# Performance work log

Measured on AMD Instinct MI355X. Metric: run time of the kernel, lower is better.

Reference implementation:

```python
import jax, jax.numpy as jnp
import numpy as np

B, S, D, H = 2, 2048, 1024, 16
DK = D // H

def setup_inputs() -> dict:
    key = jax.random.key(0)
    k_x, k_q, k_k, k_v, k_o = jax.random.split(key, 5)
    return {
        "x": jax.random.normal(k_x, (B, S, D), dtype=jnp.float32),
        "wq": jax.random.normal(k_q, (D, D), dtype=jnp.float32) * 0.02,
        "wk": jax.random.normal(k_k, (D, D), dtype=jnp.float32) * 0.02,
        "wv": jax.random.normal(k_v, (D, D), dtype=jnp.float32) * 0.02,
        "wo": jax.random.normal(k_o, (D, D), dtype=jnp.float32) * 0.02,
    }

def reference(x, wq, wk, wv, wo):
    b, s, d = x.shape
    # project and split heads: [b, h, s, dk]
    q = (x @ wq).reshape(b, s, H, DK).transpose(0, 2, 1, 3)
    k = (x @ wk).reshape(b, s, H, DK).transpose(0, 2, 1, 3)
    v = (x @ wv).reshape(b, s, H, DK).transpose(0, 2, 1, 3)
    scores = jnp.einsum("bhqd,bhkd->bhqk", q, k) / jnp.sqrt(jnp.float32(DK))
    causal = jnp.tril(jnp.ones((s, s), dtype=bool))  # True = keep
    scores = jnp.where(causal, scores, jnp.finfo(scores.dtype).min)
    probs = jax.nn.softmax(scores, axis=-1)  # dropout pdrop=0.0 -> identity
    out = jnp.einsum("bhqk,bhkd->bhqd", probs, v)
    out = out.transpose(0, 2, 1, 3).reshape(b, s, d)
    return out @ wo
```

## Files before the change

kernel.cpp:

```cpp
#include <hip/hip_runtime.h>
#include <hip/hip_bf16.h>

typedef short s16x8 __attribute__((ext_vector_type(8)));
typedef float f32x4 __attribute__((ext_vector_type(4)));
typedef float f32x16 __attribute__((ext_vector_type(16)));
typedef unsigned short u16x4 __attribute__((ext_vector_type(4)));
typedef unsigned int u32x4 __attribute__((ext_vector_type(4)));

#define D_MODEL 1024
#define N_HEAD  16
#define D_HEAD  64
#define SEQ     2048
#define NBATCH  2

#if __has_builtin(__builtin_amdgcn_exp2f)
#define EXP2(x) __builtin_amdgcn_exp2f(x)
#else
#define EXP2(x) exp2f(x)
#endif

#define GLOAD_LDS16(g, l) \
    __builtin_amdgcn_global_load_lds((const __attribute__((address_space(1))) void*)(g), \
                                     (__attribute__((address_space(3))) void*)(l), 16, 0, 0)

__device__ __forceinline__ unsigned short f2bf(float f) {
    union { float f; unsigned int u; } v; v.f = f;
    unsigned int r = v.u + 0x7FFFu + ((v.u >> 16) & 1u);
    return (unsigned short)(r >> 16);
}

__device__ __forceinline__ float bf2f(unsigned short u) {
    union { unsigned int u; float f; } v; v.u = ((unsigned int)u) << 16;
    return v.f;
}

__device__ __forceinline__ unsigned cvtpk_bf16(float lo, float hi) {
    unsigned r;
    asm("v_cvt_pk_bf16_f32 %0, %1, %2" : "=v"(r) : "v"(lo), "v"(hi));
    return r;
}


__global__ __launch_bounds__(256) void cvt_x_kernel(const float* __restrict__ in,
                                                    unsigned short* __restrict__ out) {
    int i = (blockIdx.x * 256 + threadIdx.x) * 4;
    float4 v = *reinterpret_cast<const float4*>(in + i);
    u16x4 o;
    o.x = f2bf(v.x); o.y = f2bf(v.y); o.z = f2bf(v.z); o.w = f2bf(v.w);
    *reinterpret_cast<u16x4*>(out + i) = o;
}

__global__ __launch_bounds__(256) void cvt_w_kernel(
    const float* __restrict__ w0, const float* __restrict__ w1,
    const float* __restrict__ w2, const float* __restrict__ w3,
    unsigned short* __restrict__ o0, unsigned short* __restrict__ o1,
    unsigned short* __restrict__ o2, unsigned short* __restrict__ o3)
{
    __shared__ unsigned short T[64][72];
    const int t = threadIdx.x;
    const int z = blockIdx.y;
    const float* w = (z == 0) ? w0 : (z == 1) ? w1 : (z == 2) ? w2 : w3;
    unsigned short* wt = (z == 0) ? o0 : (z == 1) ? o1 : (z == 2) ? o2 : o3;
    const int k0 = ((int)blockIdx.x & 15) * 64, n0 = ((int)blockIdx.x >> 4) * 64;
#pragma unroll
    for (int i = 0; i < 4; ++i) {
        int k = (t >> 4) + i * 16;
        int n = (t & 15) * 4;
        float4 v = *reinterpret_cast<const float4*>(&w[(k0 + k) * 1024 + n0 + n]);
        T[n + 0][k] = f2bf(v.x); T[n + 1][k] = f2bf(v.y);
        T[n + 2][k] = f2bf(v.z); T[n + 3][k] = f2bf(v.w);
    }
    __syncthreads();
#pragma unroll
    for (int i = 0; i < 2; ++i) {
        int n = (t >> 3) + i * 32;
        int kc = (t & 7) * 8;
        *reinterpret_cast<s16x8*>(&wt[(n0 + n) * 1024 + k0 + kc]) =
            *reinterpret_cast<const s16x8*>(&T[n][kc]);
    }
}


__global__ __launch_bounds__(256, 3) void gemm_qkv_kernel(
    const unsigned short* __restrict__ xb,
    const unsigned short* __restrict__ wqt, const unsigned short* __restrict__ wkt,
    const unsigned short* __restrict__ wvt,
    unsigned short* __restrict__ Qb, unsigned short* __restrict__ Kb,
    unsigned short* __restrict__ Vtb)
{
    __shared__ unsigned short As[128 * 64];
    __shared__ unsigned short Bs[128 * 64];
    const int t = threadIdx.x, lane = t & 63, wid = t >> 6;
    const int wr = wid >> 1, wc = wid & 1;
    const int l15 = lane & 15, l4 = lane >> 4;
    const int m0 = blockIdx.y * 128, n0 = blockIdx.x * 128;
    const int z = blockIdx.z;
    const unsigned short* Bt = (z == 0) ? wqt : (z == 1) ? wkt : wvt;

    const int srow = t >> 3;
    const int srcoff = (((t & 7) ^ (srow & 7)) << 3);
    const unsigned short* Ab = xb + (size_t)(m0 + srow) * D_MODEL + srcoff;
    const unsigned short* Bb = Bt + (size_t)(n0 + srow) * D_MODEL + srcoff;
    const int ldsoff = t * 8;
    const int rsw = l15 & 7;

    f32x4 acc[4][4];
#pragma unroll
    for (int m = 0; m < 4; ++m)
#pragma unroll
        for (int n = 0; n < 4; ++n) acc[m][n] = (f32x4){0.f, 0.f, 0.f, 0.f};

    for (int k0 = 0; k0 < D_MODEL; k0 += 64) {
        __syncthreads();
#pragma unroll
        for (int i = 0; i < 4; ++i) {
            GLOAD_LDS16(Ab + (size_t)(i * 32) * D_MODEL + k0, &As[i * 2048 + ldsoff]);
            GLOAD_LDS16(Bb + (size_t)(i * 32) * D_MODEL + k0, &Bs[i * 2048 + ldsoff]);
        }
        __syncthreads();

#pragma unroll
        for (int ks = 0; ks < 2; ++ks) {
            const int csl = ks * 4 + l4;
            s16x8 af[4], bfr[4];
#pragma unroll
            for (int m = 0; m < 4; ++m)
                af[m] = *reinterpret_cast<const s16x8*>(
                    &As[(wr * 64 + m * 16 + l15) * 64 + ((csl ^ rsw) << 3)]);
#pragma unroll
            for (int n = 0; n < 4; ++n)
                bfr[n] = *reinterpret_cast<const s16x8*>(
                    &Bs[(wc * 64 + n * 16 + l15) * 64 + ((csl ^ rsw) << 3)]);
            __builtin_amdgcn_s_setprio(1);
#pragma unroll
            for (int m = 0; m < 4; ++m)
#pragma unroll
                for (int n = 0; n < 4; ++n)
                    acc[m][n] = __builtin_amdgcn_mfma_f32_16x16x32_bf16(af[m], bfr[n], acc[m][n], 0, 0, 0);
            __builtin_amdgcn_s_setprio(0);
        }
    }

    const int rb = m0 + wr * 64, cb = n0 + wc * 64;
    if (z == 2) {
#pragma unroll
        for (int m = 0; m < 4; ++m) {
            int row = rb + m * 16 + l4 * 4;
            int b = row >> 11, s = row & 2047;
#pragma unroll
            for (int n = 0; n < 4; ++n) {
                int col = cb + n * 16 + l15;
                int h = col >> 6, dk = col & 63;
                u16x4 o;
                o.x = f2bf(acc[m][n][0]); o.y = f2bf(acc[m][n][1]);
                o.z = f2bf(acc[m][n][2]); o.w = f2bf(acc[m][n][3]);
                *reinterpret_cast<u16x4*>(&Vtb[(((b * N_HEAD + h) * D_HEAD + dk) << 11) + s]) = o;
            }
        }
    } else {
        unsigned short* C = (z == 0) ? Qb : Kb;
        const float alpha = (z == 0) ? 0.18033688011112042f : 1.0f;
#pragma unroll
        for (int m = 0; m < 4; ++m)
#pragma unroll
            for (int n = 0; n < 4; ++n)
#pragma unroll
                for (int r = 0; r < 4; ++r)
                    C[(rb + m * 16 + l4 * 4 + r) * D_MODEL + cb + n * 16 + l15] =
                        f2bf(acc[m][n][r] * alpha);
    }
}


__global__ __launch_bounds__(256, 3) void gemm_out_kernel(
    const unsigned short* __restrict__ attnb, const unsigned short* __restrict__ wot,
    float* __restrict__ out)
{
    __shared__ unsigned short As[128 * 64];
    __shared__ unsigned short Bs[64 * 64];
    const int t = threadIdx.x, lane = t & 63, wid = t >> 6;
    const int wr = wid >> 1, wc = wid & 1;
    const int l15 = lane & 15, l4 = lane >> 4;
    const int m0 = blockIdx.y * 128, n0 = blockIdx.x * 64;

    const int srow = t >> 3;
    const int srcoff = (((t & 7) ^ (srow & 7)) << 3);
    const unsigned short* Ab = attnb + (size_t)(m0 + srow) * D_MODEL + srcoff;
    const unsigned short* Bb = wot + (size_t)(n0 + srow) * D_MODEL + srcoff;
    const int ldsoff = t * 8;
    const int rsw = l15 & 7;

    f32x4 acc[4][2];
#pragma unroll
    for (int m = 0; m < 4; ++m)
#pragma unroll
        for (int n = 0; n < 2; ++n) acc[m][n] = (f32x4){0.f, 0.f, 0.f, 0.f};

    for (int k0 = 0; k0 < D_MODEL; k0 += 64) {
        __syncthreads();
#pragma unroll
        for (int i = 0; i < 4; ++i)
            GLOAD_LDS16(Ab + (size_t)(i * 32) * D_MODEL + k0, &As[i * 2048 + ldsoff]);
#pragma unroll
        for (int i = 0; i < 2; ++i)
            GLOAD_LDS16(Bb + (size_t)(i * 32) * D_MODEL + k0, &Bs[i * 2048 + ldsoff]);
        __syncthreads();

#pragma unroll
        for (int ks = 0; ks < 2; ++ks) {
            const int csl = ks * 4 + l4;
            s16x8 af[4], bfr[2];
#pragma unroll
            for (int m = 0; m < 4; ++m)
                af[m] = *reinterpret_cast<const s16x8*>(
                    &As[(wr * 64 + m * 16 + l15) * 64 + ((csl ^ rsw) << 3)]);
#pragma unroll
            for (int n = 0; n < 2; ++n)
                bfr[n] = *reinterpret_cast<const s16x8*>(
                    &Bs[(wc * 32 + n * 16 + l15) * 64 + ((csl ^ rsw) << 3)]);
            __builtin_amdgcn_s_setprio(1);
#pragma unroll
            for (int m = 0; m < 4; ++m)
#pragma unroll
                for (int n = 0; n < 2; ++n)
                    acc[m][n] = __builtin_amdgcn_mfma_f32_16x16x32_bf16(af[m], bfr[n], acc[m][n], 0, 0, 0);
            __builtin_amdgcn_s_setprio(0);
        }
    }

    const int rb = m0 + wr * 64, cb = n0 + wc * 32;
#pragma unroll
    for (int m = 0; m < 4; ++m)
#pragma unroll
        for (int n = 0; n < 2; ++n)
#pragma unroll
            for (int r = 0; r < 4; ++r)
                out[(rb + m * 16 + l4 * 4 + r) * D_MODEL + cb + n * 16 + l15] = acc[m][n][r];
}


__global__ __launch_bounds__(256, 4) void attn_kernel(
    const unsigned short* __restrict__ Qb, const unsigned short* __restrict__ Kb,
    const unsigned short* __restrict__ Vtb, unsigned short* __restrict__ Ob,
    unsigned short* __restrict__ Opart, float* __restrict__ larr)
{
    __shared__ unsigned short SMEM[8192];
    __shared__ unsigned short SMEMV[8192];

    const int t = threadIdx.x;
    const int lane = t & 63, wid = t >> 6;
    const int l31 = lane & 31, l5 = lane >> 5;

    const int bid = blockIdx.x;
    int bh, s, ta, tb; bool split;
    if (bid < 512) {
        bh = bid >> 4;
        int r = bid & 15;
        s = 8 + (r >> 1);
        int c = r & 1;
        int half = s + 1;
        ta = c * half; tb = ta + half;
        split = true;
    } else {
        int u = bid - 512;
        bh = u >> 3; s = u & 7;
        ta = 0; tb = 2 * (s + 1);
        split = false;
    }
    const int b = bh >> 4, h = bh & 15;
    const int q0 = s << 7;
    const int qw = q0 + wid * 32;
    const int qrow = qw + l31;

    s16x8 qf[4];
#pragma unroll
    for (int ks = 0; ks < 4; ++ks)
        qf[ks] = *reinterpret_cast<const s16x8*>(
            &Qb[(size_t)(b * SEQ + qrow) * D_MODEL + h * D_HEAD + ks * 16 + l5 * 8]);

    f32x16 oacc[2];
#pragma unroll
    for (int d = 0; d < 2; ++d)
#pragma unroll
        for (int r = 0; r < 16; ++r) oacc[d][r] = 0.f;
    float lrun = 0.f;

    const int stK = (wid & 1) * 32;
    const int srow = lane >> 3;
    const int scol = ((lane & 7) ^ srow) * 8;
    const unsigned short* kgb = Kb + (size_t)(b * SEQ + stK + srow) * D_MODEL + h * D_HEAD + scol;
    const unsigned short* vgb = Vtb + ((size_t)(bh * D_HEAD + stK + srow) << 11) + scol;
    const int swz = (l31 & 7);

#define STAGE(bufidx, kvbase) do { \
    if (wid < 2) { \
        const unsigned short* kg = kgb + (size_t)(kvbase) * D_MODEL; \
        _Pragma("unroll") \
        for (int i_ = 0; i_ < 4; ++i_) \
            GLOAD_LDS16(kg + (size_t)(i_ * 8) * D_MODEL, &SMEM[(bufidx) * 4096 + (stK + i_ * 8) * 64]); \
    } else { \
        const unsigned short* vg = vgb + (kvbase); \
        _Pragma("unroll") \
        for (int i_ = 0; i_ < 4; ++i_) \
            GLOAD_LDS16(vg + ((size_t)(i_ * 8) << 11), &SMEMV[(bufidx) * 4096 + (stK + i_ * 8) * 64]); \
    } } while (0)

    STAGE(0, ta * 64);

    for (int ti = ta; ti < tb; ++ti) {
        const int cur = (ti - ta) & 1;
        const int kv0 = ti * 64;
        __builtin_amdgcn_sched_barrier(0);
        asm volatile("s_waitcnt vmcnt(0)" ::: "memory");
        __builtin_amdgcn_s_barrier();
        if (ti + 1 < tb) STAGE(cur ^ 1, (ti + 1) * 64);
        __builtin_amdgcn_sched_barrier(0);

        if (kv0 > qw + 31) continue;

        const unsigned short* KsC = &SMEM[cur * 4096];
        const unsigned short* VsC = &SMEMV[cur * 4096];

        f32x16 sacc[2];
#pragma unroll
        for (int kvsub = 0; kvsub < 2; ++kvsub) {
            const bool active = (kv0 + kvsub * 32 <= qw + 31);
            if (active) {
#pragma unroll
                for (int r = 0; r < 16; ++r) sacc[kvsub][r] = -8.0f;
                __builtin_amdgcn_s_setprio(1);
#pragma unroll
                for (int ks = 0; ks < 4; ++ks) {
                    s16x8 kf = *reinterpret_cast<const s16x8*>(
                        &KsC[(kvsub * 32 + l31) * 64 + (((2 * ks + l5) ^ swz) * 8)]);
                    sacc[kvsub] = __builtin_amdgcn_mfma_f32_32x32x16_bf16(kf, qf[ks], sacc[kvsub], 0, 0, 0);
                }
                __builtin_amdgcn_s_setprio(0);
                if (kv0 + kvsub * 32 + 31 > qw) {
                    int kvbase = kv0 + kvsub * 32 + 4 * l5;
#pragma unroll
                    for (int r = 0; r < 16; ++r) {
                        int kvg = kvbase + (r & 3) + 8 * (r >> 2);
                        sacc[kvsub][r] = (kvg > qrow) ? -1e30f : sacc[kvsub][r];
                    }
                }
#pragma unroll
                for (int r = 0; r < 16; ++r) sacc[kvsub][r] = EXP2(sacc[kvsub][r]);
            } else {
#pragma unroll
                for (int r = 0; r < 16; ++r) sacc[kvsub][r] = 0.f;
            }
        }

        float sred[16];
#pragma unroll
        for (int r = 0; r < 16; ++r) sred[r] = sacc[0][r] + sacc[1][r];
#pragma unroll
        for (int sj = 8; sj >= 1; sj >>= 1)
#pragma unroll
            for (int r = 0; r < 8; ++r)
                if (r < sj) sred[r] += sred[r + sj];
        lrun += sred[0] + __shfl_xor(sred[0], 32);

#pragma unroll
        for (int ks = 0; ks < 4; ++ks) {
            if (kv0 + (ks >> 1) * 32 > qw + 31) continue;
            const int kvsub = ks >> 1, bo = (ks & 1) * 8;
            unsigned a0 = cvtpk_bf16(sacc[kvsub][bo + 0], sacc[kvsub][bo + 1]);
            unsigned a1 = cvtpk_bf16(sacc[kvsub][bo + 2], sacc[kvsub][bo + 3]);
            unsigned a2 = cvtpk_bf16(sacc[kvsub][bo + 4], sacc[kvsub][bo + 5]);
            unsigned a3 = cvtpk_bf16(sacc[kvsub][bo + 6], sacc[kvsub][bo + 7]);
            asm volatile("v_permlane32_swap_b32 %0, %1" : "+v"(a0), "+v"(a2));
            asm volatile("v_permlane32_swap_b32 %0, %1" : "+v"(a1), "+v"(a3));
            u32x4 pw; pw.x = a0; pw.y = a1; pw.z = a2; pw.w = a3;
            s16x8 pf = __builtin_bit_cast(s16x8, pw);
            __builtin_amdgcn_s_setprio(1);
#pragma unroll
            for (int dsub = 0; dsub < 2; ++dsub) {
                s16x8 vf = *reinterpret_cast<const s16x8*>(
                    &VsC[(dsub * 32 + l31) * 64 + (((2 * ks + l5) ^ swz) * 8)]);
                oacc[dsub] = __builtin_amdgcn_mfma_f32_32x32x16_bf16(vf, pf, oacc[dsub], 0, 0, 0);
            }
            __builtin_amdgcn_s_setprio(0);
        }
    }
    __syncthreads();

    float inv = split ? 1.0f : (1.0f / lrun);
    const int orow = wid * 32 + l31;
#pragma unroll
    for (int dsub = 0; dsub < 2; ++dsub)
#pragma unroll
        for (int a = 0; a < 4; ++a) {
            unsigned w0 = cvtpk_bf16(oacc[dsub][4 * a + 0] * inv, oacc[dsub][4 * a + 1] * inv);
            unsigned w1 = cvtpk_bf16(oacc[dsub][4 * a + 2] * inv, oacc[dsub][4 * a + 3] * inv);
            int slot = (4 * dsub + a) ^ (orow & 7);
            uint2 pr; pr.x = w0; pr.y = w1;
            *reinterpret_cast<uint2*>(&SMEM[orow * 64 + slot * 8 + l5 * 4]) = pr;
        }
    __syncthreads();
    if (split) {
        unsigned short* Op = Opart + (size_t)bid * 8192;
#pragma unroll
        for (int i = 0; i < 4; ++i) {
            int g = i * 256 + t;
            int row = g >> 3, c16 = g & 7;
            int cs = (c16 ^ (row & 7)) * 8;
            *reinterpret_cast<s16x8*>(&Op[row * 64 + c16 * 8]) =
                *reinterpret_cast<const s16x8*>(&SMEM[row * 64 + cs]);
        }
        if (l5 == 0) larr[bid * 128 + orow] = lrun;
    } else {
#pragma unroll
        for (int i = 0; i < 4; ++i) {
            int g = i * 256 + t;
            int row = g >> 3, c16 = g & 7;
            int cs = (c16 ^ (row & 7)) * 8;
            s16x8 v = *reinterpret_cast<const s16x8*>(&SMEM[row * 64 + cs]);
            *reinterpret_cast<s16x8*>(
                &Ob[(size_t)(b * SEQ + q0 + row) * D_MODEL + h * D_HEAD + c16 * 8]) = v;
        }
    }
#undef STAGE
}


__global__ __launch_bounds__(256) void combine_kernel(
    const unsigned short* __restrict__ Opart, const float* __restrict__ larr,
    unsigned short* __restrict__ Ob)
{
    const int u = blockIdx.x;
    const int bh = u >> 3, s = (u & 7) + 8;
    const int b = bh >> 4, h = bh & 15;
    const int slotA = u * 2, slotB = slotA + 1;
    const unsigned short* A = Opart + (size_t)slotA * 8192;
    const unsigned short* B = Opart + (size_t)slotB * 8192;
    const int t = threadIdx.x;
#pragma unroll
    for (int i = 0; i < 4; ++i) {
        int g = i * 256 + t;
        int row = g >> 3, c8 = (g & 7) * 8;
        float inv = 1.0f / (larr[slotA * 128 + row] + larr[slotB * 128 + row]);
        s16x8 va = *reinterpret_cast<const s16x8*>(&A[row * 64 + c8]);
        s16x8 vb = *reinterpret_cast<const s16x8*>(&B[row * 64 + c8]);
        union { s16x8 v; unsigned short e[8]; } o;
#pragma unroll
        for (int j = 0; j < 8; ++j)
            o.e[j] = f2bf((bf2f((unsigned short)va[j]) + bf2f((unsigned short)vb[j])) * inv);
        *reinterpret_cast<s16x8*>(
            &Ob[(size_t)(b * SEQ + s * 128 + row) * D_MODEL + h * D_HEAD + c8]) = o.v;
    }
}


extern "C" void kernel_launch(void* const* d_in, const int* in_sizes, int n_in,
                              void* d_out, int out_size, void* d_ws, size_t ws_size,
                              hipStream_t stream) {
    (void)in_sizes; (void)n_in; (void)out_size; (void)ws_size;
    const float* x  = (const float*)d_in[0];
    const float* wq = (const float*)d_in[1];
    const float* wk = (const float*)d_in[2];
    const float* wv = (const float*)d_in[3];
    const float* wo = (const float*)d_in[4];
    float* out = (float*)d_out;

    char* ws = (char*)d_ws;
    unsigned short* xb  = (unsigned short*)(ws);
    unsigned short* wqt = (unsigned short*)(ws + (8u  << 20));
    unsigned short* wkt = (unsigned short*)(ws + (10u << 20));
    unsigned short* wvt = (unsigned short*)(ws + (12u << 20));
    unsigned short* wot = (unsigned short*)(ws + (14u << 20));
    unsigned short* Qb  = (unsigned short*)(ws + (16u << 20));
    unsigned short* Kb  = (unsigned short*)(ws + (24u << 20));
    unsigned short* Vtb = (unsigned short*)(ws + (32u << 20));
    unsigned short* Ob  = (unsigned short*)(ws + (40u << 20));
    unsigned short* Opart = xb;
    float*          larr  = (float*)wqt;

    hipLaunchKernelGGL(cvt_x_kernel, dim3(4096), dim3(256), 0, stream, x, xb);
    hipLaunchKernelGGL(cvt_w_kernel, dim3(256, 4), dim3(256), 0, stream,
                       wq, wk, wv, wo, wqt, wkt, wvt, wot);

    hipLaunchKernelGGL(gemm_qkv_kernel, dim3(8, 32, 3), dim3(256), 0, stream,
                       xb, wqt, wkt, wvt, Qb, Kb, Vtb);
    hipLaunchKernelGGL(attn_kernel, dim3(768), dim3(256), 0, stream,
                       Qb, Kb, Vtb, Ob, Opart, larr);
    hipLaunchKernelGGL(combine_kernel, dim3(256), dim3(256), 0, stream, Opart, larr, Ob);
    hipLaunchKernelGGL(gemm_out_kernel, dim3(16, 32), dim3(256), 0, stream, Ob, wot, out);
}
```

Measured before the change: 102.4 us.

## Rebalance causal attention work split with chunks capped at twelve KV tiles

Replaces the old split, where query blocks 8-15 were cut in half and blocks 0-7 ran whole, with a lookup-table schedule. Every work item now covers at most 12 KV tiles, so query blocks 6-11 are split two ways and 12-15 three ways. Work items are ordered largest first and interleaved across batch-heads, which should cut tail imbalance across CUs. The cost is more blocks, more partial outputs to write, and a combine kernel that now merges up to three partials per block, with the l array moved to a different workspace region.

```diff
diff --git a/kernel.cpp b/kernel.cpp
--- a/kernel.cpp
+++ b/kernel.cpp
@@ -39,6 +39,11 @@
     asm("v_cvt_pk_bf16_f32 %0, %1, %2" : "=v"(r) : "v"(lo), "v"(hi));
     return r;
 }
+
+__device__ const unsigned char T_S[30] = {5,6,7,8,9,10,11,11,12,12,13,13,14,14,15,15,
+                                          4,10, 3,9,15, 2,8,14, 1,7,13, 0,6,12};
+__device__ const unsigned char T_C[30] = {0,0,0,0,0,0,0,1,0,1,0,1,0,1,0,1,
+                                          0,1, 0,1,2, 0,1,2, 0,1,2, 0,1,2};
 
 
 __global__ __launch_bounds__(256) void cvt_x_kernel(const float* __restrict__ in,
@@ -252,21 +257,14 @@
     const int l31 = lane & 31, l5 = lane >> 5;
 
     const int bid = blockIdx.x;
-    int bh, s, ta, tb; bool split;
-    if (bid < 512) {
-        bh = bid >> 4;
-        int r = bid & 15;
-        s = 8 + (r >> 1);
-        int c = r & 1;
-        int half = s + 1;
-        ta = c * half; tb = ta + half;
-        split = true;
-    } else {
-        int u = bid - 512;
-        bh = u >> 3; s = u & 7;
-        ta = 0; tb = 2 * (s + 1);
-        split = false;
-    }
+    const int type = bid >> 5, bh = bid & 31;
+    const int s = T_S[type], c = T_C[type];
+    const int ta = c * 12;
+    const int tbf = 2 * (s + 1);
+    const int tb = (ta + 12 < tbf) ? ta + 12 : tbf;
+    const bool split = (s >= 6);
+    const int slot = bh * 24 + ((s < 12) ? (s - 6) * 2 + c : 12 + (s - 12) * 3 + c);
+
     const int b = bh >> 4, h = bh & 15;
     const int q0 = s << 7;
     const int qw = q0 + wid * 32;
@@ -394,13 +392,13 @@
         for (int a = 0; a < 4; ++a) {
             unsigned w0 = cvtpk_bf16(oacc[dsub][4 * a + 0] * inv, oacc[dsub][4 * a + 1] * inv);
             unsigned w1 = cvtpk_bf16(oacc[dsub][4 * a + 2] * inv, oacc[dsub][4 * a + 3] * inv);
-            int slot = (4 * dsub + a) ^ (orow & 7);
+            int slt = (4 * dsub + a) ^ (orow & 7);
             uint2 pr; pr.x = w0; pr.y = w1;
-            *reinterpret_cast<uint2*>(&SMEM[orow * 64 + slot * 8 + l5 * 4]) = pr;
+            *reinterpret_cast<uint2*>(&SMEM[orow * 64 + slt * 8 + l5 * 4]) = pr;
         }
     __syncthreads();
     if (split) {
-        unsigned short* Op = Opart + (size_t)bid * 8192;
+        unsigned short* Op = Opart + (size_t)slot * 8192;
 #pragma unroll
         for (int i = 0; i < 4; ++i) {
             int g = i * 256 + t;
@@ -409,7 +407,7 @@
             *reinterpret_cast<s16x8*>(&Op[row * 64 + c16 * 8]) =
                 *reinterpret_cast<const s16x8*>(&SMEM[row * 64 + cs]);
         }
-        if (l5 == 0) larr[bid * 128 + orow] = lrun;
+        if (l5 == 0) larr[slot * 128 + orow] = lrun;
     } else {
 #pragma unroll
         for (int i = 0; i < 4; ++i) {
@@ -430,23 +428,35 @@
     unsigned short* __restrict__ Ob)
 {
     const int u = blockIdx.x;
-    const int bh = u >> 3, s = (u & 7) + 8;
+    const int bh = u / 10, s = (u % 10) + 6;
     const int b = bh >> 4, h = bh & 15;
-    const int slotA = u * 2, slotB = slotA + 1;
-    const unsigned short* A = Opart + (size_t)slotA * 8192;
-    const unsigned short* B = Opart + (size_t)slotB * 8192;
+    const int base = bh * 24;
+    const int s0 = (s < 12) ? base + (s - 6) * 2 : base + 12 + (s - 12) * 3;
+    const int n = (s < 12) ? 2 : 3;
     const int t = threadIdx.x;
 #pragma unroll
     for (int i = 0; i < 4; ++i) {
         int g = i * 256 + t;
         int row = g >> 3, c8 = (g & 7) * 8;
-        float inv = 1.0f / (larr[slotA * 128 + row] + larr[slotB * 128 + row]);
-        s16x8 va = *reinterpret_cast<const s16x8*>(&A[row * 64 + c8]);
-        s16x8 vb = *reinterpret_cast<const s16x8*>(&B[row * 64 + c8]);
+        float lsum = larr[s0 * 128 + row] + larr[(s0 + 1) * 128 + row];
+        if (n == 3) lsum += larr[(s0 + 2) * 128 + row];
+        float inv = 1.0f / lsum;
+        float acc[8];
+        {
+            s16x8 va = *reinterpret_cast<const s16x8*>(&Opart[(size_t)s0 * 8192 + row * 64 + c8]);
+            s16x8 vb = *reinterpret_cast<const s16x8*>(&Opart[(size_t)(s0 + 1) * 8192 + row * 64 + c8]);
+#pragma unroll
+            for (int j = 0; j < 8; ++j)
+                acc[j] = bf2f((unsigned short)va[j]) + bf2f((unsigned short)vb[j]);
+            if (n == 3) {
+                s16x8 vc = *reinterpret_cast<const s16x8*>(&Opart[(size_t)(s0 + 2) * 8192 + row * 64 + c8]);
+#pragma unroll
+                for (int j = 0; j < 8; ++j) acc[j] += bf2f((unsigned short)vc[j]);
+            }
+        }
         union { s16x8 v; unsigned short e[8]; } o;
 #pragma unroll
-        for (int j = 0; j < 8; ++j)
-            o.e[j] = f2bf((bf2f((unsigned short)va[j]) + bf2f((unsigned short)vb[j])) * inv);
+        for (int j = 0; j < 8; ++j) o.e[j] = f2bf(acc[j] * inv);
         *reinterpret_cast<s16x8*>(
             &Ob[(size_t)(b * SEQ + s * 128 + row) * D_MODEL + h * D_HEAD + c8]) = o.v;
     }
@@ -475,7 +485,7 @@
     unsigned short* Vtb = (unsigned short*)(ws + (32u << 20));
     unsigned short* Ob  = (unsigned short*)(ws + (40u << 20));
     unsigned short* Opart = xb;
-    float*          larr  = (float*)wqt;
+    float*          larr  = (float*)wvt;
 
     hipLaunchKernelGGL(cvt_x_kernel, dim3(4096), dim3(256), 0, stream, x, xb);
     hipLaunchKernelGGL(cvt_w_kernel, dim3(256, 4), dim3(256), 0, stream,
@@ -483,8 +493,8 @@
 
     hipLaunchKernelGGL(gemm_qkv_kernel, dim3(8, 32, 3), dim3(256), 0, stream,
                        xb, wqt, wkt, wvt, Qb, Kb, Vtb);
-    hipLaunchKernelGGL(attn_kernel, dim3(768), dim3(256), 0, stream,
+    hipLaunchKernelGGL(attn_kernel, dim3(960), dim3(256), 0, stream,
                        Qb, Kb, Vtb, Ob, Opart, larr);
-    hipLaunchKernelGGL(combine_kernel, dim3(256), dim3(256), 0, stream, Opart, larr, Ob);
+    hipLaunchKernelGGL(combine_kernel, dim3(320), dim3(256), 0, stream, Opart, larr, Ob);
     hipLaunchKernelGGL(gemm_out_kernel, dim3(16, 32), dim3(256), 0, stream, Ob, wot, out);
 }
```

Measured after the change: 98.32 us (median of 2 runs). -4.0%, faster.
